# Kernel tuning notes

Measured on AMD Instinct MI355X. Metric: run time of the kernel, lower is better.

The kernel has to match this reference:

```python
import jax, jax.numpy as jnp
import numpy as np

N_EXPERTS = 20
DIM = 32
EPS = 1e-12  # F.normalize eps


def setup_inputs() -> dict:
    key = jax.random.key(0)
    k_x, k_pos, k_w1, k_b1, k_w0, k_b0 = jax.random.split(key, 6)
    B = 131072
    bound = 1.0 / np.sqrt(DIM)  # torch Linear default init range
    return {
        "x": jax.random.normal(k_x, (B, DIM), dtype=jnp.float32),
        "W1": jax.random.uniform(k_w1, (N_EXPERTS, DIM, DIM), jnp.float32, -bound, bound),
        "b1": jax.random.uniform(k_b1, (N_EXPERTS, DIM), jnp.float32, -bound, bound),
        "W0": jax.random.uniform(k_w0, (N_EXPERTS, DIM, DIM), jnp.float32, -bound, bound),
        "b0": jax.random.uniform(k_b0, (N_EXPERTS, DIM), jnp.float32, -bound, bound),
        "pos": jax.random.randint(k_pos, (B,), 0, N_EXPERTS, dtype=jnp.int64),
    }


def reference(x, W1, b1, W0, b0, pos):
    # Gather per-sample expert weights (routing): [B, DIM, DIM] / [B, DIM]
    W1g, b1g = W1[pos], b1[pos]
    W0g, b0g = W0[pos], b0[pos]
    # fc1: y = x @ W1^T + b1 (torch Linear convention, W is [out, in])
    h = jnp.einsum("bi,boi->bo", x, W1g) + b1g
    # fc0
    out = jnp.einsum("bi,boi->bo", h, W0g) + b0g
    # F.normalize(dim=-1): x / max(||x||_2, eps)
    norm = jnp.sqrt(jnp.sum(out * out, axis=-1, keepdims=True))
    return out / jnp.maximum(norm, EPS)
```

## Files before the change

kernel.cpp:

```cpp
#include <hip/hip_runtime.h>
#include <stdint.h>

#define N_EXPERTS 20
#define DIM 32
#define SPB 256
#define MAIN_T 256
#define MROW 40
#define MAX_TILES 48

using frag_ab = __attribute__((ext_vector_type(8))) short;
using frag_cd = __attribute__((ext_vector_type(4))) float;

static __device__ __forceinline__ short f2bf(float f) {
    union { float f; uint32_t u; } v; v.f = f;
    uint32_t u = v.u;
    return (short)(uint16_t)((u + 0x7FFFu + ((u >> 16) & 1u)) >> 16);
}

__global__ __launch_bounds__(256) void k_prep(
    const float* __restrict__ W1, const float* __restrict__ b1,
    const float* __restrict__ W0, const float* __restrict__ b0,
    unsigned short* __restrict__ Mbf, float* __restrict__ cvec)
{
    __shared__ float s1[1024], s0[1024];
    int e = blockIdx.x, t = threadIdx.x;
    const float* w1 = W1 + e * 1024;
    const float* w0 = W0 + e * 1024;
    for (int i = t; i < 1024; i += 256) { s1[i] = w1[i]; s0[i] = w0[i]; }
    __syncthreads();
    for (int idx = t; idx < 1024; idx += 256) {
        int o = idx >> 5, i = idx & 31;
        float s = 0.f;
        #pragma unroll
        for (int k = 0; k < 32; k++) s += s0[o*32 + k] * s1[k*32 + i];
        Mbf[e*1024 + o*32 + i] = (unsigned short)f2bf(s);
    }
    if (t < DIM) {
        float s = b0[e*32 + t];
        #pragma unroll
        for (int k = 0; k < 32; k++) s += s0[t*32 + k] * b1[e*32 + k];
        cvec[e*32 + t] = s;
    }
}

__global__ __launch_bounds__(MAIN_T) void k_moe(
    const float* __restrict__ x, const int* __restrict__ pos,
    const unsigned short* __restrict__ Mbf, const float* __restrict__ cvec,
    float* __restrict__ out, int B)
{
    __shared__ unsigned short Ms[N_EXPERTS * 32 * MROW];
    __shared__ float cs[N_EXPERTS * 32];
    __shared__ int hist[N_EXPERTS];
    __shared__ int lstart[N_EXPERTS + 1];
    __shared__ int cursor[N_EXPERTS];
    __shared__ int lidx[SPB];
    __shared__ int tileE[MAX_TILES], tileB[MAX_TILES];
    __shared__ int ntiles;

    int t = threadIdx.x;
    int base = blockIdx.x * SPB;
    int S = min(SPB, B - base);
    if (S <= 0) return;

    if (t < N_EXPERTS) hist[t] = 0;
    __syncthreads();

    {
        const uint32_t* msrc = (const uint32_t*)Mbf;
        uint32_t* mdst = (uint32_t*)Ms;
        for (int d = t; d < N_EXPERTS * 512; d += MAIN_T) {
            int e = d >> 9, rem = d & 511;
            int n = rem >> 4, c = rem & 15;
            mdst[e * (32 * MROW / 2) + n * (MROW / 2) + c] = msrc[d];
        }
        for (int i = t; i < N_EXPERTS * 32; i += MAIN_T) cs[i] = cvec[i];
    }
    int my_e = -1;
    if (t < S) {
        my_e = pos[base + t];
        atomicAdd(&hist[my_e], 1);
    }
    __syncthreads();

    int lane = t & 63, wave = t >> 6;

    if (wave == 0) {
        int e = lane;
        int h = (e < N_EXPERTS) ? hist[e] : 0;
        int s = h;
        #pragma unroll
        for (int d = 1; d < 32; d <<= 1) { int v = __shfl_up(s, d); if (lane >= d) s += v; }
        int pre = s - h;
        int ntl = (h + 15) >> 4;
        int ts = ntl;
        #pragma unroll
        for (int d = 1; d < 32; d <<= 1) { int v = __shfl_up(ts, d); if (lane >= d) ts += v; }
        int tpre = ts - ntl;
        if (e < N_EXPERTS) {
            lstart[e] = pre; cursor[e] = pre;
            for (int k = 0; k < ntl; k++) { tileE[tpre + k] = e; tileB[tpre + k] = pre + 16 * k; }
            if (e == N_EXPERTS - 1) { lstart[N_EXPERTS] = pre + h; ntiles = tpre + ntl; }
        }
    }
    __syncthreads();

    if (t < S) {
        int slot = atomicAdd(&cursor[my_e], 1);
        lidx[slot] = t;
    }
    __syncthreads();

    int nt = ntiles;
    int n = lane & 15, q = lane >> 4;

    int ti = wave;
    float4 xa, xb;
    int cur_e = 0, cur_tb = 0, cur_bend = 0;
    if (ti < nt) {
        cur_e = tileE[ti]; cur_tb = tileB[ti]; cur_bend = lstart[cur_e + 1];
        int slot = min(cur_tb + n, cur_bend - 1);
        int l = lidx[slot];
        const float* xr = x + (size_t)(base + l) * 32 + q * 8;
        xa = *(const float4*)xr; xb = *(const float4*)(xr + 4);
    }
    for (; ti < nt; ti += 4) {
        int e = cur_e, tb = cur_tb, bend = cur_bend;
        float4 a0 = xa, a1 = xb;
        int tj = ti + 4;
        if (tj < nt) {
            cur_e = tileE[tj]; cur_tb = tileB[tj]; cur_bend = lstart[cur_e + 1];
            int slot = min(cur_tb + n, cur_bend - 1);
            int l = lidx[slot];
            const float* xr = x + (size_t)(base + l) * 32 + q * 8;
            xa = *(const float4*)xr; xb = *(const float4*)(xr + 4);
        }

        const unsigned short* mrow = Ms + e * 32 * MROW;
        frag_ab bf0 = *(const frag_ab*)(mrow + n * MROW + q * 8);
        frag_ab bf1 = *(const frag_ab*)(mrow + (n + 16) * MROW + q * 8);
        float c0 = cs[e * 32 + n];
        float c1 = cs[e * 32 + 16 + n];

        frag_ab af;
        af[0] = f2bf(a0.x); af[1] = f2bf(a0.y); af[2] = f2bf(a0.z); af[3] = f2bf(a0.w);
        af[4] = f2bf(a1.x); af[5] = f2bf(a1.y); af[6] = f2bf(a1.z); af[7] = f2bf(a1.w);

        frag_cd z = {0.f, 0.f, 0.f, 0.f};
        frag_cd d0 = __builtin_amdgcn_mfma_f32_16x16x32_bf16(af, bf0, z, 0, 0, 0);
        frag_cd d1 = __builtin_amdgcn_mfma_f32_16x16x32_bf16(af, bf1, z, 0, 0, 0);

        #pragma unroll
        for (int r = 0; r < 4; r++) {
            int os = tb + q * 4 + r;
            float v0 = d0[r] + c0;
            float v1 = d1[r] + c1;
            float ss = v0 * v0 + v1 * v1;
            ss += __shfl_xor(ss, 1);
            ss += __shfl_xor(ss, 2);
            ss += __shfl_xor(ss, 4);
            ss += __shfl_xor(ss, 8);
            float sc = rsqrtf(fmaxf(ss, 1e-24f));
            if (os < bend) {
                int lo = lidx[os];
                float* op = out + (size_t)(base + lo) * 32;
                op[n]      = v0 * sc;
                op[16 + n] = v1 * sc;
            }
        }
    }
}

extern "C" void kernel_launch(void* const* d_in, const int* in_sizes, int n_in,
                              void* d_out, int out_size, void* d_ws, size_t ws_size,
                              hipStream_t stream) {
    const float* x  = (const float*)d_in[0];
    const float* W1 = (const float*)d_in[1];
    const float* b1 = (const float*)d_in[2];
    const float* W0 = (const float*)d_in[3];
    const float* b0 = (const float*)d_in[4];
    const int*  pos = (const int*)d_in[5];
    float* out = (float*)d_out;
    int B = in_sizes[0] / DIM;

    char* ws = (char*)d_ws;
    unsigned short* Mbf = (unsigned short*)ws;
    float* cvec = (float*)(ws + (size_t)N_EXPERTS * 1024 * 2);

    k_prep<<<N_EXPERTS, 256, 0, stream>>>(W1, b1, W0, b0, Mbf, cvec);
    int nblk = (B + SPB - 1) / SPB;
    k_moe<<<nblk, MAIN_T, 0, stream>>>(x, pos, Mbf, cvec, out, B);
}
```

Baseline: 89.84 us.

## Replace sorted MFMA tiles with per-thread scalar matvec over LDS expert weights

Drops the per-block histogram, expert sort and MFMA tile dispatch. Each thread now loads its own sample's 32 floats, computes the 32x32 matvec with its expert's bf16 fused matrix from LDS using scalar FMAs, normalizes, and writes 8 float4s. This removes several syncs, the scatter indirection and the gather of x, and gives contiguous vectorized loads and stores. The cost is about 1024 FMAs per thread, LDS reads that differ per lane, and higher register pressure from holding the input and 32 accumulators.

```diff
diff --git a/kernel.cpp b/kernel.cpp
--- a/kernel.cpp
+++ b/kernel.cpp
@@ -3,18 +3,19 @@
 
 #define N_EXPERTS 20
 #define DIM 32
-#define SPB 256
-#define MAIN_T 256
-#define MROW 40
-#define MAX_TILES 48
-
-using frag_ab = __attribute__((ext_vector_type(8))) short;
-using frag_cd = __attribute__((ext_vector_type(4))) float;
+#define TMOE 512
+#define MSTR 1032
 
 static __device__ __forceinline__ short f2bf(float f) {
     union { float f; uint32_t u; } v; v.f = f;
     uint32_t u = v.u;
     return (short)(uint16_t)((u + 0x7FFFu + ((u >> 16) & 1u)) >> 16);
+}
+static __device__ __forceinline__ float bfl(uint32_t u) {
+    union { uint32_t u; float f; } v; v.u = u << 16; return v.f;
+}
+static __device__ __forceinline__ float bfh(uint32_t u) {
+    union { uint32_t u; float f; } v; v.u = u & 0xFFFF0000u; return v.f;
 }
 
 __global__ __launch_bounds__(256) void k_prep(
@@ -43,130 +44,73 @@
     }
 }
 
-__global__ __launch_bounds__(MAIN_T) void k_moe(
+__global__ __launch_bounds__(TMOE) void k_moe(
     const float* __restrict__ x, const int* __restrict__ pos,
     const unsigned short* __restrict__ Mbf, const float* __restrict__ cvec,
     float* __restrict__ out, int B)
 {
-    __shared__ unsigned short Ms[N_EXPERTS * 32 * MROW];
-    __shared__ float cs[N_EXPERTS * 32];
-    __shared__ int hist[N_EXPERTS];
-    __shared__ int lstart[N_EXPERTS + 1];
-    __shared__ int cursor[N_EXPERTS];
-    __shared__ int lidx[SPB];
-    __shared__ int tileE[MAX_TILES], tileB[MAX_TILES];
-    __shared__ int ntiles;
+    __shared__ unsigned short Ms[N_EXPERTS * MSTR];
+    __shared__ float cs[N_EXPERTS * DIM];
 
     int t = threadIdx.x;
-    int base = blockIdx.x * SPB;
-    int S = min(SPB, B - base);
-    if (S <= 0) return;
+    int s = blockIdx.x * TMOE + t;
 
-    if (t < N_EXPERTS) hist[t] = 0;
-    __syncthreads();
+    float4 xv[8];
+    int e = 0;
+    bool live = (s < B);
+    if (live) {
+        const float4* xp = (const float4*)(x + (size_t)s * 32);
+        #pragma unroll
+        for (int i = 0; i < 8; i++) xv[i] = xp[i];
+        e = pos[s];
+    }
 
     {
-        const uint32_t* msrc = (const uint32_t*)Mbf;
-        uint32_t* mdst = (uint32_t*)Ms;
-        for (int d = t; d < N_EXPERTS * 512; d += MAIN_T) {
-            int e = d >> 9, rem = d & 511;
-            int n = rem >> 4, c = rem & 15;
-            mdst[e * (32 * MROW / 2) + n * (MROW / 2) + c] = msrc[d];
+        const uint4* msrc = (const uint4*)Mbf;
+        for (int i = t; i < N_EXPERTS * 128; i += TMOE) {
+            int ee = i >> 7, r = i & 127;
+            uint4 v = msrc[i];
+            *(uint4*)&Ms[ee * MSTR + r * 8] = v;
         }
-        for (int i = t; i < N_EXPERTS * 32; i += MAIN_T) cs[i] = cvec[i];
-    }
-    int my_e = -1;
-    if (t < S) {
-        my_e = pos[base + t];
-        atomicAdd(&hist[my_e], 1);
+        for (int i = t; i < N_EXPERTS * DIM; i += TMOE) cs[i] = cvec[i];
     }
     __syncthreads();
+    if (!live) return;
 
-    int lane = t & 63, wave = t >> 6;
+    const unsigned short* M = Ms + e * MSTR;
+    const float* c = cs + e * 32;
 
-    if (wave == 0) {
-        int e = lane;
-        int h = (e < N_EXPERTS) ? hist[e] : 0;
-        int s = h;
+    float acc[32];
+    #pragma unroll 4
+    for (int o = 0; o < 32; o++) {
+        const uint4* mp = (const uint4*)(M + o * 32);
+        float a = c[o];
         #pragma unroll
-        for (int d = 1; d < 32; d <<= 1) { int v = __shfl_up(s, d); if (lane >= d) s += v; }
-        int pre = s - h;
-        int ntl = (h + 15) >> 4;
-        int ts = ntl;
-        #pragma unroll
-        for (int d = 1; d < 32; d <<= 1) { int v = __shfl_up(ts, d); if (lane >= d) ts += v; }
-        int tpre = ts - ntl;
-        if (e < N_EXPERTS) {
-            lstart[e] = pre; cursor[e] = pre;
-            for (int k = 0; k < ntl; k++) { tileE[tpre + k] = e; tileB[tpre + k] = pre + 16 * k; }
-            if (e == N_EXPERTS - 1) { lstart[N_EXPERTS] = pre + h; ntiles = tpre + ntl; }
+        for (int kk = 0; kk < 4; kk++) {
+            uint4 m = mp[kk];
+            float4 x0 = xv[2*kk], x1 = xv[2*kk + 1];
+            a += bfl(m.x) * x0.x + bfh(m.x) * x0.y
+               + bfl(m.y) * x0.z + bfh(m.y) * x0.w
+               + bfl(m.z) * x1.x + bfh(m.z) * x1.y
+               + bfl(m.w) * x1.z + bfh(m.w) * x1.w;
         }
+        acc[o] = a;
     }
-    __syncthreads();
 
-    if (t < S) {
-        int slot = atomicAdd(&cursor[my_e], 1);
-        lidx[slot] = t;
-    }
-    __syncthreads();
+    float ss = 0.f;
+    #pragma unroll
+    for (int o = 0; o < 32; o++) ss += acc[o] * acc[o];
+    float sc = rsqrtf(fmaxf(ss, 1e-24f));
 
-    int nt = ntiles;
-    int n = lane & 15, q = lane >> 4;
-
-    int ti = wave;
-    float4 xa, xb;
-    int cur_e = 0, cur_tb = 0, cur_bend = 0;
-    if (ti < nt) {
-        cur_e = tileE[ti]; cur_tb = tileB[ti]; cur_bend = lstart[cur_e + 1];
-        int slot = min(cur_tb + n, cur_bend - 1);
-        int l = lidx[slot];
-        const float* xr = x + (size_t)(base + l) * 32 + q * 8;
-        xa = *(const float4*)xr; xb = *(const float4*)(xr + 4);
-    }
-    for (; ti < nt; ti += 4) {
-        int e = cur_e, tb = cur_tb, bend = cur_bend;
-        float4 a0 = xa, a1 = xb;
-        int tj = ti + 4;
-        if (tj < nt) {
-            cur_e = tileE[tj]; cur_tb = tileB[tj]; cur_bend = lstart[cur_e + 1];
-            int slot = min(cur_tb + n, cur_bend - 1);
-            int l = lidx[slot];
-            const float* xr = x + (size_t)(base + l) * 32 + q * 8;
-            xa = *(const float4*)xr; xb = *(const float4*)(xr + 4);
-        }
-
-        const unsigned short* mrow = Ms + e * 32 * MROW;
-        frag_ab bf0 = *(const frag_ab*)(mrow + n * MROW + q * 8);
-        frag_ab bf1 = *(const frag_ab*)(mrow + (n + 16) * MROW + q * 8);
-        float c0 = cs[e * 32 + n];
-        float c1 = cs[e * 32 + 16 + n];
-
-        frag_ab af;
-        af[0] = f2bf(a0.x); af[1] = f2bf(a0.y); af[2] = f2bf(a0.z); af[3] = f2bf(a0.w);
-        af[4] = f2bf(a1.x); af[5] = f2bf(a1.y); af[6] = f2bf(a1.z); af[7] = f2bf(a1.w);
-
-        frag_cd z = {0.f, 0.f, 0.f, 0.f};
-        frag_cd d0 = __builtin_amdgcn_mfma_f32_16x16x32_bf16(af, bf0, z, 0, 0, 0);
-        frag_cd d1 = __builtin_amdgcn_mfma_f32_16x16x32_bf16(af, bf1, z, 0, 0, 0);
-
-        #pragma unroll
-        for (int r = 0; r < 4; r++) {
-            int os = tb + q * 4 + r;
-            float v0 = d0[r] + c0;
-            float v1 = d1[r] + c1;
-            float ss = v0 * v0 + v1 * v1;
-            ss += __shfl_xor(ss, 1);
-            ss += __shfl_xor(ss, 2);
-            ss += __shfl_xor(ss, 4);
-            ss += __shfl_xor(ss, 8);
-            float sc = rsqrtf(fmaxf(ss, 1e-24f));
-            if (os < bend) {
-                int lo = lidx[os];
-                float* op = out + (size_t)(base + lo) * 32;
-                op[n]      = v0 * sc;
-                op[16 + n] = v1 * sc;
-            }
-        }
+    float4* op = (float4*)(out + (size_t)s * 32);
+    #pragma unroll
+    for (int k = 0; k < 8; k++) {
+        float4 v;
+        v.x = acc[4*k + 0] * sc;
+        v.y = acc[4*k + 1] * sc;
+        v.z = acc[4*k + 2] * sc;
+        v.w = acc[4*k + 3] * sc;
+        op[k] = v;
     }
 }
 
@@ -187,6 +131,6 @@
     float* cvec = (float*)(ws + (size_t)N_EXPERTS * 1024 * 2);
 
     k_prep<<<N_EXPERTS, 256, 0, stream>>>(W1, b1, W0, b0, Mbf, cvec);
-    int nblk = (B + SPB - 1) / SPB;
-    k_moe<<<nblk, MAIN_T, 0, stream>>>(x, pos, Mbf, cvec, out, B);
+    int nblk = (B + TMOE - 1) / TMOE;
+    k_moe<<<nblk, TMOE, 0, stream>>>(x, pos, Mbf, cvec, out, B);
 }
```

After: 90.41 us. Within noise of the previous version (+0.6%).
